# Kernel tuning notes

Measured on AMD Instinct MI355X. Metric: run time of the kernel, lower is better.

The kernel has to match this reference:

```python
import jax, jax.numpy as jnp
import numpy as np

B, S, D, H, DH, K, M = 2, 1024, 1024, 16, 64, 32, 8192
LN_EPS = 1e-5


def _ln(x, g, b):
    mu = jnp.mean(x, axis=-1, keepdims=True)
    var = jnp.var(x, axis=-1, keepdims=True)
    return (x - mu) * jax.lax.rsqrt(var + LN_EPS) * g + b


def _split_heads(t):  # [B,S,H*DH] -> [B,H,S,DH]
    return t.reshape(B, S, H, DH).transpose(0, 2, 1, 3)


def setup_inputs() -> dict:
    key = jax.random.key(0)
    ks = jax.random.split(key, 10)
    sd = 1.0 / np.sqrt(D)
    return {
        "x": jax.random.normal(ks[0], (B, S, D), jnp.float32),
        "mem_k_db": jax.random.normal(ks[1], (B, M, D), jnp.float32),
        "mem_v_db": jax.random.normal(ks[2], (B, M, D), jnp.float32),
        "g_val": jax.random.uniform(ks[3], (H,), jnp.float32),
        "ln1_g": jnp.ones((D,), jnp.float32),
        "ln1_b": jnp.zeros((D,), jnp.float32),
        "W_attn": jax.random.normal(ks[4], (D, 3 * D), jnp.float32) * sd,
        "b_attn": jnp.zeros((3 * D,), jnp.float32),
        "W_proj": jax.random.normal(ks[5], (D, D), jnp.float32) * sd,
        "b_proj": jnp.zeros((D,), jnp.float32),
        "ln2_g": jnp.ones((D,), jnp.float32),
        "ln2_b": jnp.zeros((D,), jnp.float32),
        "W_fc": jax.random.normal(ks[6], (D, 4 * D), jnp.float32) * sd,
        "b_fc": jnp.zeros((4 * D,), jnp.float32),
        "W_out": jax.random.normal(ks[7], (4 * D, D), jnp.float32) / np.sqrt(4 * D),
        "b_out": jnp.zeros((D,), jnp.float32),
    }


def reference(x, mem_k_db, mem_v_db, g_val, ln1_g, ln1_b, W_attn, b_attn,
              W_proj, b_proj, ln2_g, ln2_b, W_fc, b_fc, W_out, b_out):
    residual = x
    h = _ln(x, ln1_g, ln1_b)
    qkv = h @ W_attn + b_attn                       # [B,S,3D]
    q_f, k_f, v_f = jnp.split(qkv, 3, axis=-1)      # each [B,S,D]
    q = _split_heads(q_f)                           # [B,H,S,DH]
    k = _split_heads(k_f)
    v = _split_heads(v_f)

    # --- kNN memory search (non-per-head path): l2-normalized concat-head query ---
    sq = q_f / jnp.linalg.norm(q_f, axis=-1, keepdims=True).clip(1e-12)
    sims = jnp.einsum('bsd,bmd->bsm', sq, mem_k_db)          # [B,S,M]
    _, idx = jax.lax.top_k(sims, K)                          # [B,S,K]
    idx_e = idx[..., None]                                   # [B,S,K,1]
    mem_k = jnp.take_along_axis(mem_k_db[:, None], idx_e, axis=2)  # [B,S,K,D]
    mem_v = jnp.take_along_axis(mem_v_db[:, None], idx_e, axis=2)  # [B,S,K,D]
    # split memory into heads: [B,S,K,H*DH] -> [B,H,S,K,DH]
    mem_k = mem_k.reshape(B, S, K, H, DH).transpose(0, 3, 1, 2, 4)
    mem_v = mem_v.reshape(B, S, K, H, DH).transpose(0, 3, 1, 2, 4)

    inv_sqrt_dh = 1.0 / np.sqrt(DH)
    mem_w = jnp.einsum('bhid,bhijd->bhij', q, mem_k) * inv_sqrt_dh   # [B,H,S,K]

    std_w = jnp.einsum('bhid,bhjd->bhij', q, k) * inv_sqrt_dh        # [B,H,S,S]
    causal = jnp.tril(jnp.ones((S, S), bool))
    mask_val = jnp.finfo(std_w.dtype).min
    std_w = jnp.where(causal, std_w, mask_val)

    all_w = jax.nn.softmax(jnp.concatenate([mem_w, std_w], axis=-1), axis=-1)
    mem_attn, local_attn = all_w[..., :K], all_w[..., K:]

    local_out = jnp.einsum('bhij,bhjd->bhid', local_attn, v)
    mem_out = jnp.einsum('bhij,bhijd->bhid', mem_attn, mem_v)

    g = g_val.reshape(1, H, 1, 1)
    attn_out = (1.0 - g) * local_out + g * mem_out           # [B,H,S,DH]
    attn_out = attn_out.transpose(0, 2, 1, 3).reshape(B, S, D)
    attn_out = attn_out @ W_proj + b_proj

    h = attn_out + residual
    residual2 = h
    h = _ln(h, ln2_g, ln2_b)
    h = jax.nn.gelu(h @ W_fc + b_fc, approximate=True) @ W_out + b_out
    return residual2 + h
```

## Files before the change

### kernel.cpp

```cpp
#include <hip/hip_runtime.h>
#include <stdint.h>

#define DEV static __device__ __forceinline__

typedef __attribute__((ext_vector_type(8))) __bf16 bf16x8;
typedef __attribute__((ext_vector_type(4))) float f32x4;

DEV float bf2f(uint32_t u) {
  union { uint32_t i; float f; } v; v.i = u << 16; return v.f;
}
DEV uint16_t f2bf(float f) {
  union { float f; uint32_t i; } v; v.f = f;
  uint32_t x = v.i;
  return (uint16_t)((x + 0x7FFFu + ((x >> 16) & 1u)) >> 16);
}
DEV f32x4 mfma16(bf16x8 a, bf16x8 b, f32x4 c) {
  return __builtin_amdgcn_mfma_f32_16x16x32_bf16(a, b, c, 0, 0, 0);
}
DEV bf16x8 as_bf16x8(uint4 u) { return __builtin_bit_cast(bf16x8, u); }

DEV void gload16(const uint16_t* __restrict__ g, uint16_t* l) {
  __builtin_amdgcn_global_load_lds(
      (const __attribute__((address_space(1))) uint32_t*)g,
      (__attribute__((address_space(3))) uint32_t*)l, 16, 0, 0);
}

DEV float gelu_tanh(float x) {
  float x3 = x * x * x;
  float u = 0.7978845608028654f * (x + 0.044715f * x3);
  return 0.5f * x * (1.0f + tanhf(u));
}
DEV unsigned mono_key(float f) {
  union { float f; uint32_t u; } v; v.f = f;
  return (v.u & 0x80000000u) ? ~v.u : (v.u | 0x80000000u);
}

__global__ __launch_bounds__(256) void k_transpose_cast(
    const float* __restrict__ in, uint16_t* __restrict__ out,
    uint16_t* __restrict__ outlo, int R, int C) {
  __shared__ float tile[32][33];
  int c0 = blockIdx.x * 32, r0 = blockIdx.y * 32;
  int tx = threadIdx.x % 32, ty = threadIdx.x / 32;
  for (int i = 0; i < 32; i += 8)
    tile[ty + i][tx] = in[(size_t)(r0 + ty + i) * C + c0 + tx];
  __syncthreads();
  for (int i = 0; i < 32; i += 8) {
    float v = tile[tx][ty + i];
    uint16_t hi = f2bf(v);
    out[(size_t)(c0 + ty + i) * R + r0 + tx] = hi;
    if (outlo)
      outlo[(size_t)(c0 + ty + i) * R + r0 + tx] = f2bf(v - bf2f(hi));
  }
}

__global__ __launch_bounds__(256) void k_cast_bf16(
    const float* __restrict__ in, uint16_t* __restrict__ out, long n) {
  long i = ((long)blockIdx.x * 256 + threadIdx.x) * 4;
  if (i >= n) return;
  float4 v = *(const float4*)(in + i);
  uint2 pk;
  pk.x = (uint32_t)f2bf(v.x) | ((uint32_t)f2bf(v.y) << 16);
  pk.y = (uint32_t)f2bf(v.z) | ((uint32_t)f2bf(v.w) << 16);
  *(uint2*)(out + i) = pk;
}

__global__ __launch_bounds__(256) void k_layernorm(
    const float* __restrict__ x, const float* __restrict__ g,
    const float* __restrict__ bb, uint16_t* __restrict__ out,
    uint16_t* __restrict__ outlo) {
  int row = blockIdx.x;
  const float* xr = x + (size_t)row * 1024;
  int c = threadIdx.x * 4;
  float4 v = *(const float4*)(xr + c);
  float s = v.x + v.y + v.z + v.w;
  float s2 = v.x * v.x + v.y * v.y + v.z * v.z + v.w * v.w;
  for (int off = 32; off; off >>= 1) {
    s += __shfl_down(s, off, 64);
    s2 += __shfl_down(s2, off, 64);
  }
  __shared__ float ps[4], qs[4];
  int lane = threadIdx.x & 63, wv = threadIdx.x >> 6;
  if (!lane) { ps[wv] = s; qs[wv] = s2; }
  __syncthreads();
  float S = ps[0] + ps[1] + ps[2] + ps[3];
  float S2 = qs[0] + qs[1] + qs[2] + qs[3];
  float mu = S * (1.f / 1024.f);
  float var = S2 * (1.f / 1024.f) - mu * mu;
  float rinv = rsqrtf(var + 1e-5f);
  const float* vv = (const float*)&v;
  uint16_t o[4], ol[4];
#pragma unroll
  for (int j = 0; j < 4; j++) {
    float y = (vv[j] - mu) * rinv * g[c + j] + bb[c + j];
    o[j] = f2bf(y);
    ol[j] = f2bf(y - bf2f(o[j]));
  }
  uint2 pk;
  pk.x = (uint32_t)o[0] | ((uint32_t)o[1] << 16);
  pk.y = (uint32_t)o[2] | ((uint32_t)o[3] << 16);
  *(uint2*)(out + (size_t)row * 1024 + c) = pk;
  if (outlo) {
    pk.x = (uint32_t)ol[0] | ((uint32_t)ol[1] << 16);
    pk.y = (uint32_t)ol[2] | ((uint32_t)ol[3] << 16);
    *(uint2*)(outlo + (size_t)row * 1024 + c) = pk;
  }
}

template <int EPI>
__global__ __launch_bounds__(256) void k_gemm3(
    const uint16_t* __restrict__ A, int lda,
    const uint16_t* __restrict__ Bt, int ldb,
    void* __restrict__ Cout, int ldc,
    const float* __restrict__ bias,
    const float* __restrict__ resid,
    int Kc) {
  const int m0 = blockIdx.y * 128, n0 = blockIdx.x * 128;
  const int kt0 = (EPI & 16) ? blockIdx.z * Kc : 0;
  __shared__ __align__(16) uint16_t As[128 * 32];
  __shared__ __align__(16) uint16_t Bs[128 * 32];
  const int t = threadIdx.x, l = t & 63, w = t >> 6;
  const int wr = w >> 1, wc = w & 1;
  const int lg = l >> 4, lr = l & 15;

  const int g1 = w * 64 + l;
  const int r1 = g1 >> 2, c1 = g1 & 3;
  const int r2 = r1 + 64;
  const int cs1 = c1 ^ ((r1 >> 1) & 3);
  const int cs2 = c1 ^ ((r2 >> 1) & 3);
  const uint16_t* pa1 = A + (size_t)(m0 + r1) * lda + kt0 + cs1 * 8;
  const uint16_t* pa2 = A + (size_t)(m0 + r2) * lda + kt0 + cs2 * 8;
  const uint16_t* pb1 = Bt + (size_t)(n0 + r1) * ldb + kt0 + cs1 * 8;
  const uint16_t* pb2 = Bt + (size_t)(n0 + r2) * ldb + kt0 + cs2 * 8;
  uint16_t* la1 = As + w * 512;
  uint16_t* la2 = As + 2048 + w * 512;
  uint16_t* lb1 = Bs + w * 512;
  uint16_t* lb2 = Bs + 2048 + w * 512;

  int offA[4], offB[4];
#pragma unroll
  for (int i = 0; i < 4; i++) {
    int row = wr * 64 + i * 16 + lr;
    offA[i] = (row * 4 + (lg ^ ((row >> 1) & 3))) * 8;
  }
#pragma unroll
  for (int j = 0; j < 4; j++) {
    int row = wc * 64 + j * 16 + lr;
    offB[j] = (row * 4 + (lg ^ ((row >> 1) & 3))) * 8;
  }

  f32x4 acc[4][4] = {};
  for (int kt = 0; kt < Kc; kt += 32) {
    __syncthreads();
    gload16(pa1, la1); gload16(pa2, la2);
    gload16(pb1, lb1); gload16(pb2, lb2);
    pa1 += 32; pa2 += 32; pb1 += 32; pb2 += 32;
    __syncthreads();
    bf16x8 af[4], bfr[4];
#pragma unroll
    for (int i = 0; i < 4; i++) af[i] = as_bf16x8(*(const uint4*)(As + offA[i]));
#pragma unroll
    for (int j = 0; j < 4; j++) bfr[j] = as_bf16x8(*(const uint4*)(Bs + offB[j]));
#pragma unroll
    for (int i = 0; i < 4; i++)
#pragma unroll
      for (int j = 0; j < 4; j++)
        acc[i][j] = mfma16(af[i], bfr[j], acc[i][j]);
  }
  const size_t zoff = (EPI & 16) ? (size_t)blockIdx.z * gridDim.y * 128 * ldc : 0;
#pragma unroll
  for (int i = 0; i < 4; i++)
#pragma unroll
    for (int j = 0; j < 4; j++)
#pragma unroll
      for (int r = 0; r < 4; r++) {
        int row = m0 + wr * 64 + i * 16 + lg * 4 + r;
        int col = n0 + wc * 64 + j * 16 + lr;
        float v = acc[i][j][r];
        if constexpr (EPI & 16) {
          ((float*)Cout)[zoff + (size_t)row * ldc + col] = v;
        } else {
          if constexpr (EPI & 1) v += bias[col];
          if constexpr (EPI & 4) v = gelu_tanh(v);
          if constexpr (EPI & 2) v += resid[(size_t)row * ldc + col];
          if constexpr (EPI & 8)
            ((uint16_t*)Cout)[(size_t)row * ldc + col] = f2bf(v);
          else
            ((float*)Cout)[(size_t)row * ldc + col] = v;
        }
      }
}

__global__ __launch_bounds__(256) void k_gemm_split3(
    const uint16_t* __restrict__ Ah, const uint16_t* __restrict__ Al, int lda,
    const uint16_t* __restrict__ Bh, const uint16_t* __restrict__ Bl, int ldb,
    uint16_t* __restrict__ Ch, uint16_t* __restrict__ Cl, int ldc,
    const float* __restrict__ bias, int Kd) {
  const int m0 = blockIdx.y * 128, n0 = blockIdx.x * 128;
  __shared__ __align__(16) uint16_t Ahs[128 * 32];
  __shared__ __align__(16) uint16_t Als[128 * 32];
  __shared__ __align__(16) uint16_t Bhs[128 * 32];
  __shared__ __align__(16) uint16_t Bls[128 * 32];
  const int t = threadIdx.x, l = t & 63, w = t >> 6;
  const int wr = w >> 1, wc = w & 1;
  const int lg = l >> 4, lr = l & 15;

  const int g1 = w * 64 + l;
  const int r1 = g1 >> 2, c1 = g1 & 3;
  const int r2 = r1 + 64;
  const int cs1 = c1 ^ ((r1 >> 1) & 3);
  const int cs2 = c1 ^ ((r2 >> 1) & 3);
  const size_t ao1 = (size_t)(m0 + r1) * lda + cs1 * 8;
  const size_t ao2 = (size_t)(m0 + r2) * lda + cs2 * 8;
  const size_t bo1 = (size_t)(n0 + r1) * ldb + cs1 * 8;
  const size_t bo2 = (size_t)(n0 + r2) * ldb + cs2 * 8;
  const uint16_t* pah1 = Ah + ao1; const uint16_t* pah2 = Ah + ao2;
  const uint16_t* pal1 = Al + ao1; const uint16_t* pal2 = Al + ao2;
  const uint16_t* pbh1 = Bh + bo1; const uint16_t* pbh2 = Bh + bo2;
  const uint16_t* pbl1 = Bl + bo1; const uint16_t* pbl2 = Bl + bo2;
  uint16_t* lah1 = Ahs + w * 512; uint16_t* lah2 = Ahs + 2048 + w * 512;
  uint16_t* lal1 = Als + w * 512; uint16_t* lal2 = Als + 2048 + w * 512;
  uint16_t* lbh1 = Bhs + w * 512; uint16_t* lbh2 = Bhs + 2048 + w * 512;
  uint16_t* lbl1 = Bls + w * 512; uint16_t* lbl2 = Bls + 2048 + w * 512;

  int offA[4], offB[4];
#pragma unroll
  for (int i = 0; i < 4; i++) {
    int row = wr * 64 + i * 16 + lr;
    offA[i] = (row * 4 + (lg ^ ((row >> 1) & 3))) * 8;
  }
#pragma unroll
  for (int j = 0; j < 4; j++) {
    int row = wc * 64 + j * 16 + lr;
    offB[j] = (row * 4 + (lg ^ ((row >> 1) & 3))) * 8;
  }

  f32x4 acc[4][4] = {};
  for (int kt = 0; kt < Kd; kt += 32) {
    __syncthreads();
    gload16(pah1, lah1); gload16(pah2, lah2);
    gload16(pal1, lal1); gload16(pal2, lal2);
    gload16(pbh1, lbh1); gload16(pbh2, lbh2);
    gload16(pbl1, lbl1); gload16(pbl2, lbl2);
    pah1 += 32; pah2 += 32; pal1 += 32; pal2 += 32;
    pbh1 += 32; pbh2 += 32; pbl1 += 32; pbl2 += 32;
    __syncthreads();
    bf16x8 ah[4], al[4], bh[4], bl[4];
#pragma unroll
    for (int i = 0; i < 4; i++) {
      ah[i] = as_bf16x8(*(const uint4*)(Ahs + offA[i]));
      al[i] = as_bf16x8(*(const uint4*)(Als + offA[i]));
    }
#pragma unroll
    for (int j = 0; j < 4; j++) {
      bh[j] = as_bf16x8(*(const uint4*)(Bhs + offB[j]));
      bl[j] = as_bf16x8(*(const uint4*)(Bls + offB[j]));
    }
#pragma unroll
    for (int i = 0; i < 4; i++)
#pragma unroll
      for (int j = 0; j < 4; j++) {
        acc[i][j] = mfma16(ah[i], bh[j], acc[i][j]);
        acc[i][j] = mfma16(ah[i], bl[j], acc[i][j]);
        acc[i][j] = mfma16(al[i], bh[j], acc[i][j]);
      }
  }
#pragma unroll
  for (int i = 0; i < 4; i++)
#pragma unroll
    for (int j = 0; j < 4; j++)
#pragma unroll
      for (int r = 0; r < 4; r++) {
        int row = m0 + wr * 64 + i * 16 + lg * 4 + r;
        int col = n0 + wc * 64 + j * 16 + lr;
        float v = acc[i][j][r] + bias[col];
        uint16_t hi = f2bf(v);
        Ch[(size_t)row * ldc + col] = hi;
        Cl[(size_t)row * ldc + col] = f2bf(v - bf2f(hi));
      }
}

template <int NP>
__global__ __launch_bounds__(256) void k_merge(
    const float* __restrict__ parts, const float* __restrict__ bias,
    const float* __restrict__ resid, float* __restrict__ out) {
  int row = blockIdx.x, c = threadIdx.x * 4;
  size_t off = (size_t)row * 1024 + c;
  float4 s = *(const float4*)(resid + off);
  float4 bv = *(const float4*)(bias + c);
  s.x += bv.x; s.y += bv.y; s.z += bv.z; s.w += bv.w;
#pragma unroll
  for (int z = 0; z < NP; z++) {
    float4 pv = *(const float4*)(parts + (size_t)z * 2048 * 1024 + off);
    s.x += pv.x; s.y += pv.y; s.z += pv.z; s.w += pv.w;
  }
  *(float4*)(out + off) = s;
}

__global__ __launch_bounds__(256) void k_topk2(
    const float* __restrict__ sims,
    const uint16_t* __restrict__ qkvh,
    const uint16_t* __restrict__ qkvl,
    const float* __restrict__ memk,
    int* __restrict__ idx_out,
    float* __restrict__ mlogh) {
  int row = blockIdx.x;
  int t = threadIdx.x;
  const float* s = sims + (size_t)row * 8192;
  unsigned key[32];
#pragma unroll
  for (int k = 0; k < 8; k++) {
    float4 v = *(const float4*)(s + t * 4 + k * 1024);
    key[k * 4 + 0] = mono_key(v.x);
    key[k * 4 + 1] = mono_key(v.y);
    key[k * 4 + 2] = mono_key(v.z);
    key[k * 4 + 3] = mono_key(v.w);
  }
  __shared__ int partial[2][4];
  __shared__ int cnt_s;
  __shared__ int sidx[40];
  __shared__ float qs[1024];
  __shared__ float hval[40][16];
  int lane = t & 63, wv = t >> 6;
  unsigned lo = 0u, hi = 0xFFFFFFFFu;
  for (int it = 0; it < 32; ++it) {
    unsigned mid = lo + ((hi - lo) >> 1);
    int c = 0;
#pragma unroll
    for (int i = 0; i < 32; i++) c += (key[i] > mid) ? 1 : 0;
    for (int off = 32; off; off >>= 1) c += __shfl_down(c, off, 64);
    if (!lane) partial[it & 1][wv] = c;
    __syncthreads();
    int tot = partial[it & 1][0] + partial[it & 1][1] +
              partial[it & 1][2] + partial[it & 1][3];
    if (tot >= 40) lo = mid + 1; else hi = mid;
  }
  unsigned T = lo;
  if (t == 0) cnt_s = 0;
  __syncthreads();
#pragma unroll
  for (int i = 0; i < 32; i++)
    if (key[i] > T) {
      int p = atomicAdd(&cnt_s, 1);
      if (p < 40) sidx[p] = t * 4 + (i >> 2) * 1024 + (i & 3);
    }
  __syncthreads();
#pragma unroll
  for (int i = 0; i < 32; i++)
    if (key[i] == T) {
      int p = atomicAdd(&cnt_s, 1);
      if (p < 40) sidx[p] = t * 4 + (i >> 2) * 1024 + (i & 3);
    }
  {
    int c4 = t * 4;
    const uint16_t* qh = qkvh + (size_t)row * 3072;
    const uint16_t* ql = qkvl + (size_t)row * 3072;
    uint2 uh = *(const uint2*)(qh + c4);
    uint2 ul = *(const uint2*)(ql + c4);
    qs[c4 + 0] = bf2f(uh.x & 0xFFFF) + bf2f(ul.x & 0xFFFF);
    qs[c4 + 1] = bf2f(uh.x >> 16) + bf2f(ul.x >> 16);
    qs[c4 + 2] = bf2f(uh.y & 0xFFFF) + bf2f(ul.y & 0xFFFF);
    qs[c4 + 3] = bf2f(uh.y >> 16) + bf2f(ul.y >> 16);
  }
  __syncthreads();
  {
    float4 qreg[4];
#pragma unroll
    for (int i = 0; i < 4; i++) qreg[i] = *(const float4*)(qs + i * 256 + lane * 4);
    for (int cc = 0; cc < 10; ++cc) {
      int c = wv * 10 + cc;
      const float* kp = memk + (size_t)sidx[c] * 1024;
#pragma unroll
      for (int i = 0; i < 4; ++i) {
        float4 kv = *(const float4*)(kp + i * 256 + lane * 4);
        float pband = kv.x * qreg[i].x + kv.y * qreg[i].y +
                      kv.z * qreg[i].z + kv.w * qreg[i].w;
        pband += __shfl_xor(pband, 1, 64);
        pband += __shfl_xor(pband, 2, 64);
        pband += __shfl_xor(pband, 4, 64);
        pband += __shfl_xor(pband, 8, 64);
        if ((lane & 15) == 0) hval[c][i * 4 + (lane >> 4)] = pband;
      }
    }
  }
  __syncthreads();
  if (wv == 0) {
    float full = 0.f;
    if (t < 40) {
#pragma unroll
      for (int i = 0; i < 16; i++) full += hval[t][i];
    }
    unsigned k2 = (t < 40) ? mono_key(full) : 0u;
    unsigned lo2 = 0u, hi2 = 0xFFFFFFFFu;
    for (int it = 0; it < 32; ++it) {
      unsigned mid = lo2 + ((hi2 - lo2) >> 1);
      int c = __popcll(__ballot(k2 > mid));
      if (c >= 32) lo2 = mid + 1; else hi2 = mid;
    }
    unsigned T2 = lo2;
    unsigned long long m1 = __ballot(k2 > T2);
    unsigned long long m2 = __ballot(k2 == T2);
    int n1 = __popcll(m1);
    unsigned long long lt = ((unsigned long long)1 << t) - 1;
    int pos = 99;
    if (k2 > T2) pos = __popcll(m1 & lt);
    else if (k2 == T2 && t < 40) pos = n1 + __popcll(m2 & lt);
    if (pos < 32) {
      idx_out[(size_t)row * 32 + pos] = sidx[t];
#pragma unroll
      for (int i = 0; i < 16; i++)
        mlogh[((size_t)row * 32 + pos) * 16 + i] = hval[t][i] * 0.125f;
    }
  }
}

__global__ __launch_bounds__(256) void k_flash(
    const uint16_t* __restrict__ qkvh,
    const uint16_t* __restrict__ qkvl,
    float* __restrict__ pacc,
    float* __restrict__ pm,
    float* __restrict__ pl) {
  const int qt = 15 - blockIdx.x;
  const int chk = blockIdx.y, bh = blockIdx.z;
  const int cbase = chk * 256;
  if (cbase >= (qt + 1) * 64) return;
  const int b = bh >> 4, h = bh & 15;
  const int t = threadIdx.x, lane = t & 63, w = t >> 6;
  const int lg = lane >> 4, lr = lane & 15;
  const int q0 = qt * 64 + w * 16;
  const size_t rowb = (size_t)b * 1024;
  __shared__ __align__(16) uint16_t Kh[2][2048];
  __shared__ __align__(16) uint16_t Kl[2][2048];
  __shared__ __align__(16) uint16_t Vs[2][2048];
  __shared__ __align__(16) uint16_t Pl[4][16][40];

  bf16x8 qh[2], qlo[2];
  {
    const uint16_t* qph = qkvh + (rowb + q0 + lr) * 3072 + h * 64;
    const uint16_t* qpl = qkvl + (rowb + q0 + lr) * 3072 + h * 64;
    qh[0] = as_bf16x8(*(const uint4*)(qph + lg * 8));
    qh[1] = as_bf16x8(*(const uint4*)(qph + 32 + lg * 8));
    qlo[0] = as_bf16x8(*(const uint4*)(qpl + lg * 8));
    qlo[1] = as_bf16x8(*(const uint4*)(qpl + 32 + lg * 8));
  }
  f32x4 acc[4] = {};
  float mrow[4], lrowv[4];
#pragma unroll
  for (int r = 0; r < 4; r++) { mrow[r] = -1e30f; lrowv[r] = 0.f; }

  const int lim = min(cbase + 256, q0 + 16);
  const int blim = min(cbase + 256, (qt + 1) * 64);

  const int sr = t >> 3, sc = t & 7;
  const int scs = sc ^ (sr & 7);
  const uint16_t* gkh = qkvh + (rowb + sr) * 3072 + 1024 + h * 64 + scs * 8;
  const uint16_t* gkl = qkvl + (rowb + sr) * 3072 + 1024 + h * 64 + scs * 8;
  const uint16_t* gv  = qkvh + (rowb + sr) * 3072 + 2048 + h * 64 + scs * 8;

  {
    const size_t so = (size_t)cbase * 3072;
    gload16(gkh + so, Kh[0] + w * 512);
    gload16(gkl + so, Kl[0] + w * 512);
    gload16(gv + so, Vs[0] + w * 512);
  }
  __syncthreads();

  int cur = 0;
  for (int c0 = cbase; c0 < blim; c0 += 32) {
    if (c0 + 32 < blim) {
      const size_t so = (size_t)(c0 + 32) * 3072;
      gload16(gkh + so, Kh[cur ^ 1] + w * 512);
      gload16(gkl + so, Kl[cur ^ 1] + w * 512);
      gload16(gv + so, Vs[cur ^ 1] + w * 512);
    }
    if (c0 < lim) {
      f32x4 sf[2];
#pragma unroll
      for (int n = 0; n < 2; n++) {
        const int row = n * 16 + lr;
        const int rb = row * 64;
        const int x0 = ((lg) ^ (row & 7)) * 8;
        const int x1 = ((4 + lg) ^ (row & 7)) * 8;
        bf16x8 kh0 = as_bf16x8(*(const uint4*)(Kh[cur] + rb + x0));
        bf16x8 kh1 = as_bf16x8(*(const uint4*)(Kh[cur] + rb + x1));
        bf16x8 kl0 = as_bf16x8(*(const uint4*)(Kl[cur] + rb + x0));
        bf16x8 kl1 = as_bf16x8(*(const uint4*)(Kl[cur] + rb + x1));
        f32x4 sz = {};
        sz = mfma16(qh[0], kh0, sz);
        sz = mfma16(qh[1], kh1, sz);
        sz = mfma16(qh[0], kl0, sz);
        sz = mfma16(qh[1], kl1, sz);
        sz = mfma16(qlo[0], kh0, sz);
        sz = mfma16(qlo[1], kh1, sz);
        sf[n] = sz;
      }
      float p0[4], p1[4], alpha[4];
#pragma unroll
      for (int r = 0; r < 4; r++) {
        int rowq = q0 + lg * 4 + r;
        int col0 = c0 + lr, col1 = c0 + 16 + lr;
        float s0 = sf[0][r] * 0.125f; if (col0 > rowq) s0 = -1e30f;
        float s1 = sf[1][r] * 0.125f; if (col1 > rowq) s1 = -1e30f;
        float mt = fmaxf(s0, s1);
        mt = fmaxf(mt, __shfl_xor(mt, 1, 64));
        mt = fmaxf(mt, __shfl_xor(mt, 2, 64));
        mt = fmaxf(mt, __shfl_xor(mt, 4, 64));
        mt = fmaxf(mt, __shfl_xor(mt, 8, 64));
        float mnew = fmaxf(mrow[r], mt);
        float a = __expf(mrow[r] - mnew);
        float e0 = __expf(s0 - mnew), e1 = __expf(s1 - mnew);
        float ss = e0 + e1;
        ss += __shfl_xor(ss, 1, 64);
        ss += __shfl_xor(ss, 2, 64);
        ss += __shfl_xor(ss, 4, 64);
        ss += __shfl_xor(ss, 8, 64);
        lrowv[r] = lrowv[r] * a + ss;
        mrow[r] = mnew;
        alpha[r] = a;
        p0[r] = e0; p1[r] = e1;
      }
#pragma unroll
      for (int nv = 0; nv < 4; nv++)
#pragma unroll
        for (int r = 0; r < 4; r++) acc[nv][r] *= alpha[r];
#pragma unroll
      for (int r = 0; r < 4; r++) {
        Pl[w][lg * 4 + r][lr] = f2bf(p0[r]);
        Pl[w][lg * 4 + r][16 + lr] = f2bf(p1[r]);
      }
      bf16x8 pa = as_bf16x8(*(const uint4*)&Pl[w][lr][lg * 8]);
#pragma unroll
      for (int nv = 0; nv < 4; nv++) {
        const int col = nv * 16 + lr;
        const int cc = col >> 3, cl = col & 7;
        uint32_t vv[8];
#pragma unroll
        for (int j = 0; j < 8; j++) {
          int row = lg * 8 + j;
          vv[j] = Vs[cur][row * 64 + ((cc ^ (row & 7)) * 8 + cl)];
        }
        uint4 pk;
        pk.x = vv[0] | (vv[1] << 16);
        pk.y = vv[2] | (vv[3] << 16);
        pk.z = vv[4] | (vv[5] << 16);
        pk.w = vv[6] | (vv[7] << 16);
        acc[nv] = mfma16(pa, as_bf16x8(pk), acc[nv]);
      }
    }
    __syncthreads();
    cur ^= 1;
  }
  const size_t base = (size_t)(chk * 32 + bh) * 1024;
#pragma unroll
  for (int nv = 0; nv < 4; nv++)
#pragma unroll
    for (int r = 0; r < 4; r++) {
      int rowq = q0 + lg * 4 + r;
      pacc[(base + rowq) * 64 + nv * 16 + lr] = acc[nv][r];
    }
  if (lr == 0) {
#pragma unroll
    for (int r = 0; r < 4; r++) {
      int rowq = q0 + lg * 4 + r;
      pm[base + rowq] = mrow[r];
      pl[base + rowq] = lrowv[r];
    }
  }
}

__global__ __launch_bounds__(256) void k_memcombine(
    const float* __restrict__ mlogh,
    const float* __restrict__ memv,
    const int* __restrict__ idx,
    const float* __restrict__ pacc,
    const float* __restrict__ pm,
    const float* __restrict__ pl,
    const float* __restrict__ gval,
    uint16_t* __restrict__ attnout) {
  int row = blockIdx.x;
  int b = row >> 10, s = row & 1023;
  int qt = s >> 6;
  int nact = (qt >> 2) + 1;
  __shared__ int sidx[32];
  __shared__ float lg[16][32];
  __shared__ float sp[16][32];
  __shared__ float smx[16], ssum[16];
  __shared__ float scl[16][4], Ms[16], Ls[16];
  int t = threadIdx.x;
  if (t < 32) sidx[t] = idx[(size_t)row * 32 + t];
  {
    const float* mp = mlogh + (size_t)row * 512;
#pragma unroll
    for (int rep = 0; rep < 2; rep++) {
      int i = t + rep * 256;
      lg[i & 15][i >> 4] = mp[i];
    }
  }
  __syncthreads();
  if (t < 16) {
    float mx = -1e30f;
#pragma unroll
    for (int j = 0; j < 32; j++) mx = fmaxf(mx, lg[t][j]);
    float su = 0.f;
    for (int j = 0; j < 32; j++) {
      float e = __expf(lg[t][j] - mx);
      sp[t][j] = e; su += e;
    }
    smx[t] = mx; ssum[t] = su;
  } else if (t >= 64 && t < 80) {
    int hh = t - 64;
    float pmv[4];
    float M = -1e30f;
    for (int c = 0; c < nact; c++) {
      pmv[c] = pm[(size_t)(c * 32 + b * 16 + hh) * 1024 + s];
      M = fmaxf(M, pmv[c]);
    }
    float L = 0.f;
    for (int c = 0; c < nact; c++) {
      float e = __expf(pmv[c] - M);
      scl[hh][c] = e;
      L += e * pl[(size_t)(c * 32 + b * 16 + hh) * 1024 + s];
    }
    Ms[hh] = M; Ls[hh] = L;
  }
  __syncthreads();
#pragma unroll
  for (int cc = 0; cc < 4; cc++) {
    int col = t + cc * 256;
    int hh = col >> 6;
    float ma = 0.f;
#pragma unroll
    for (int j = 0; j < 32; j++)
      ma += sp[hh][j] * memv[((size_t)b * 8192 + sidx[j]) * 1024 + col];
    float la = 0.f;
    for (int c = 0; c < nact; c++)
      la += scl[hh][c] *
            pacc[((size_t)(c * 32 + b * 16 + hh) * 1024 + s) * 64 + (col & 63)];
    float ms = Ms[hh], ls = Ls[hh];
    float mm = smx[hh], lmm = ssum[hh];
    float Mx = fmaxf(ms, mm);
    float es = __expf(ms - Mx), em = __expf(mm - Mx);
    float L = es * ls + em * lmm;
    float gh = gval[hh];
    float o = ((1.f - gh) * es * la + gh * em * ma) / L;
    attnout[(size_t)row * 1024 + col] = f2bf(o);
  }
}

extern "C" void kernel_launch(void* const* d_in, const int* in_sizes, int n_in,
                              void* d_out, int out_size, void* d_ws, size_t ws_size,
                              hipStream_t stream) {
  (void)in_sizes; (void)n_in; (void)out_size; (void)ws_size;
  const float* x     = (const float*)d_in[0];
  const float* memkf = (const float*)d_in[1];
  const float* memvf = (const float*)d_in[2];
  const float* gval  = (const float*)d_in[3];
  const float* ln1g  = (const float*)d_in[4];
  const float* ln1b  = (const float*)d_in[5];
  const float* Wattn = (const float*)d_in[6];
  const float* battn = (const float*)d_in[7];
  const float* Wproj = (const float*)d_in[8];
  const float* bproj = (const float*)d_in[9];
  const float* ln2g  = (const float*)d_in[10];
  const float* ln2b  = (const float*)d_in[11];
  const float* Wfc   = (const float*)d_in[12];
  const float* bfc   = (const float*)d_in[13];
  const float* Wout  = (const float*)d_in[14];
  const float* bout  = (const float*)d_in[15];

  char* p = (char*)d_ws;
  auto alloc = [&](size_t bytes) -> char* {
    char* r = p;
    p += (bytes + 255) & ~(size_t)255;
    return r;
  };
  uint16_t* h_hi    = (uint16_t*)alloc(2048ull * 1024 * 2);
  uint16_t* h_lo    = (uint16_t*)alloc(2048ull * 1024 * 2);
  uint16_t* WattnTh = (uint16_t*)alloc(3072ull * 1024 * 2);
  uint16_t* WattnTl = (uint16_t*)alloc(3072ull * 1024 * 2);
  uint16_t* WprojT  = (uint16_t*)alloc(1024ull * 1024 * 2);
  uint16_t* WfcT    = (uint16_t*)alloc(4096ull * 1024 * 2);
  uint16_t* WoutT   = (uint16_t*)alloc(1024ull * 4096 * 2);
  uint16_t* memk_bf = (uint16_t*)alloc(2ull * 8192 * 1024 * 2);
  uint16_t* qkv_hi  = (uint16_t*)alloc(2048ull * 3072 * 2);
  uint16_t* qkv_lo  = (uint16_t*)alloc(2048ull * 3072 * 2);
  float*    sims    = (float*)alloc(1024ull * 8192 * 4);
  int*      idx     = (int*)alloc(2048ull * 32 * 4);
  float*    mlogh   = (float*)alloc(2048ull * 32 * 16 * 4);
  float*    pm      = (float*)alloc(4ull * 32 * 1024 * 4);
  float*    pl      = (float*)alloc(4ull * 32 * 1024 * 4);
  float*    h1      = (float*)alloc(2048ull * 1024 * 4);
  uint16_t* attn_bf = (uint16_t*)alloc(2048ull * 1024 * 2);
  uint16_t* h2_bf   = h_hi;
  float*    pacc    = sims;
  uint16_t* ffn1    = (uint16_t*)sims;
  float*    parts   = (float*)memk_bf;

  k_transpose_cast<<<dim3(96, 32), 256, 0, stream>>>(Wattn, WattnTh, WattnTl, 1024, 3072);
  k_transpose_cast<<<dim3(32, 32), 256, 0, stream>>>(Wproj, WprojT, nullptr, 1024, 1024);
  k_transpose_cast<<<dim3(128, 32), 256, 0, stream>>>(Wfc, WfcT, nullptr, 1024, 4096);
  k_transpose_cast<<<dim3(32, 128), 256, 0, stream>>>(Wout, WoutT, nullptr, 4096, 1024);
  k_cast_bf16<<<16384, 256, 0, stream>>>(memkf, memk_bf, 2l * 8192 * 1024);

  k_layernorm<<<2048, 256, 0, stream>>>(x, ln1g, ln1b, h_hi, h_lo);
  k_gemm_split3<<<dim3(24, 16), 256, 0, stream>>>(h_hi, h_lo, 1024, WattnTh, WattnTl, 1024,
                                                  qkv_hi, qkv_lo, 3072, battn, 1024);
  for (int z = 0; z < 2; ++z) {
    k_gemm3<0><<<dim3(64, 8), 256, 0, stream>>>(
        qkv_hi + (size_t)z * 1024 * 3072, 3072,
        memk_bf + (size_t)z * 8192 * 1024, 1024,
        sims, 8192, nullptr, nullptr, 1024);
    k_topk2<<<1024, 256, 0, stream>>>(
        sims,
        qkv_hi + (size_t)z * 1024 * 3072,
        qkv_lo + (size_t)z * 1024 * 3072,
        memkf + (size_t)z * 8192 * 1024,
        idx + (size_t)z * 1024 * 32,
        mlogh + (size_t)z * 1024 * 32 * 16);
  }
  k_flash<<<dim3(16, 4, 32), 256, 0, stream>>>(qkv_hi, qkv_lo, pacc, pm, pl);
  k_memcombine<<<2048, 256, 0, stream>>>(mlogh, memvf, idx, pacc, pm, pl, gval, attn_bf);
  k_gemm3<16><<<dim3(8, 16, 2), 256, 0, stream>>>(attn_bf, 1024, WprojT, 1024,
                                                  parts, 1024, nullptr, nullptr, 512);
  k_merge<2><<<2048, 256, 0, stream>>>(parts, bproj, x, h1);
  k_layernorm<<<2048, 256, 0, stream>>>(h1, ln2g, ln2b, h2_bf, nullptr);
  k_gemm3<13><<<dim3(32, 16), 256, 0, stream>>>(h2_bf, 1024, WfcT, 1024,
                                                ffn1, 4096, bfc, nullptr, 1024);
  k_gemm3<16><<<dim3(8, 16, 4), 256, 0, stream>>>(ffn1, 4096, WoutT, 4096,
                                                  parts, 1024, nullptr, nullptr, 1024);
  k_merge<4><<<2048, 256, 0, stream>>>(parts, bout, h1, (float*)d_out);
}
```

Before: 479.0 us.

## Fuse merge with LayerNorm, swizzle sims GEMM blocks, cast memory values to bf16

Three changes. The projection split-K merge now computes LayerNorm in the same kernel, which removes one launch and a reread of h1. The sims GEMM gets a grid swizzle meant to improve L2 reuse across XCDs. Memory values are cast to bf16 into the reused memk buffer so the gather in memcombine reads half the bytes, at the cost of a full 64MB-read cast pass and bf16 rounding of mem_v.

```diff
diff --git a/kernel.cpp b/kernel.cpp
--- a/kernel.cpp
+++ b/kernel.cpp
@@ -106,6 +106,48 @@
   }
 }
 
+__global__ __launch_bounds__(256) void k_merge_ln(
+    const float* __restrict__ parts, const float* __restrict__ bias,
+    const float* __restrict__ resid, const float* __restrict__ g,
+    const float* __restrict__ bb, float* __restrict__ h1out,
+    uint16_t* __restrict__ out) {
+  int row = blockIdx.x, c = threadIdx.x * 4;
+  size_t off = (size_t)row * 1024 + c;
+  float4 v = *(const float4*)(resid + off);
+  float4 bv = *(const float4*)(bias + c);
+  v.x += bv.x; v.y += bv.y; v.z += bv.z; v.w += bv.w;
+#pragma unroll
+  for (int z = 0; z < 2; z++) {
+    float4 pv = *(const float4*)(parts + (size_t)z * 2048 * 1024 + off);
+    v.x += pv.x; v.y += pv.y; v.z += pv.z; v.w += pv.w;
+  }
+  *(float4*)(h1out + off) = v;
+  float s = v.x + v.y + v.z + v.w;
+  float s2 = v.x * v.x + v.y * v.y + v.z * v.z + v.w * v.w;
+  for (int off2 = 32; off2; off2 >>= 1) {
+    s += __shfl_down(s, off2, 64);
+    s2 += __shfl_down(s2, off2, 64);
+  }
+  __shared__ float ps[4], qs[4];
+  int lane = threadIdx.x & 63, wv = threadIdx.x >> 6;
+  if (!lane) { ps[wv] = s; qs[wv] = s2; }
+  __syncthreads();
+  float S = ps[0] + ps[1] + ps[2] + ps[3];
+  float S2 = qs[0] + qs[1] + qs[2] + qs[3];
+  float mu = S * (1.f / 1024.f);
+  float var = S2 * (1.f / 1024.f) - mu * mu;
+  float rinv = rsqrtf(var + 1e-5f);
+  const float* vv = (const float*)&v;
+  uint16_t o[4];
+#pragma unroll
+  for (int j = 0; j < 4; j++)
+    o[j] = f2bf((vv[j] - mu) * rinv * g[c + j] + bb[c + j]);
+  uint2 pk;
+  pk.x = (uint32_t)o[0] | ((uint32_t)o[1] << 16);
+  pk.y = (uint32_t)o[2] | ((uint32_t)o[3] << 16);
+  *(uint2*)(out + off) = pk;
+}
+
 template <int EPI>
 __global__ __launch_bounds__(256) void k_gemm3(
     const uint16_t* __restrict__ A, int lda,
@@ -114,7 +156,17 @@
     const float* __restrict__ bias,
     const float* __restrict__ resid,
     int Kc) {
-  const int m0 = blockIdx.y * 128, n0 = blockIdx.x * 128;
+  int m0, n0;
+  if constexpr (EPI & 64) {
+    int id = blockIdx.y * gridDim.x + blockIdx.x;
+    int cpx = (gridDim.x * gridDim.y) >> 3;
+    int swz = (id & 7) * cpx + (id >> 3);
+    n0 = (swz % gridDim.x) * 128;
+    m0 = (swz / gridDim.x) * 128;
+  } else {
+    m0 = blockIdx.y * 128;
+    n0 = blockIdx.x * 128;
+  }
   const int kt0 = (EPI & 16) ? blockIdx.z * Kc : 0;
   __shared__ __align__(16) uint16_t As[128 * 32];
   __shared__ __align__(16) uint16_t Bs[128 * 32];
@@ -569,7 +621,7 @@
 
 __global__ __launch_bounds__(256) void k_memcombine(
     const float* __restrict__ mlogh,
-    const float* __restrict__ memv,
+    const uint16_t* __restrict__ memv_bf,
     const int* __restrict__ idx,
     const float* __restrict__ pacc,
     const float* __restrict__ pm,
@@ -630,7 +682,7 @@
     float ma = 0.f;
 #pragma unroll
     for (int j = 0; j < 32; j++)
-      ma += sp[hh][j] * memv[((size_t)b * 8192 + sidx[j]) * 1024 + col];
+      ma += sp[hh][j] * bf2f(memv_bf[((size_t)b * 8192 + sidx[j]) * 1024 + col]);
     float la = 0.f;
     for (int c = 0; c < nact; c++)
       la += scl[hh][c] *
@@ -693,6 +745,7 @@
   uint16_t* h2_bf   = h_hi;
   float*    pacc    = sims;
   uint16_t* ffn1    = (uint16_t*)sims;
+  uint16_t* memv_bf = memk_bf;
   float*    parts   = (float*)memk_bf;
 
   k_transpose_cast<<<dim3(96, 32), 256, 0, stream>>>(Wattn, WattnTh, WattnTl, 1024, 3072);
@@ -705,7 +758,7 @@
   k_gemm_split3<<<dim3(24, 16), 256, 0, stream>>>(h_hi, h_lo, 1024, WattnTh, WattnTl, 1024,
                                                   qkv_hi, qkv_lo, 3072, battn, 1024);
   for (int z = 0; z < 2; ++z) {
-    k_gemm3<0><<<dim3(64, 8), 256, 0, stream>>>(
+    k_gemm3<64><<<dim3(64, 8), 256, 0, stream>>>(
         qkv_hi + (size_t)z * 1024 * 3072, 3072,
         memk_bf + (size_t)z * 8192 * 1024, 1024,
         sims, 8192, nullptr, nullptr, 1024);
@@ -717,12 +770,12 @@
         idx + (size_t)z * 1024 * 32,
         mlogh + (size_t)z * 1024 * 32 * 16);
   }
+  k_cast_bf16<<<16384, 256, 0, stream>>>(memvf, memv_bf, 2l * 8192 * 1024);
   k_flash<<<dim3(16, 4, 32), 256, 0, stream>>>(qkv_hi, qkv_lo, pacc, pm, pl);
-  k_memcombine<<<2048, 256, 0, stream>>>(mlogh, memvf, idx, pacc, pm, pl, gval, attn_bf);
+  k_memcombine<<<2048, 256, 0, stream>>>(mlogh, memv_bf, idx, pacc, pm, pl, gval, attn_bf);
   k_gemm3<16><<<dim3(8, 16, 2), 256, 0, stream>>>(attn_bf, 1024, WprojT, 1024,
                                                   parts, 1024, nullptr, nullptr, 512);
-  k_merge<2><<<2048, 256, 0, stream>>>(parts, bproj, x, h1);
-  k_layernorm<<<2048, 256, 0, stream>>>(h1, ln2g, ln2b, h2_bf, nullptr);
+  k_merge_ln<<<2048, 256, 0, stream>>>(parts, bproj, x, ln2g, ln2b, h1, h2_bf);
   k_gemm3<13><<<dim3(32, 16), 256, 0, stream>>>(h2_bf, 1024, WfcT, 1024,
                                                 ffn1, 4096, bfc, nullptr, 1024);
   k_gemm3<16><<<dim3(8, 16, 4), 256, 0, stream>>>(ffn1, 4096, WoutT, 4096,
```

After: 490.5 us. 1.02x slower.
